# Performance work log

Measured on AMD Instinct MI355X. Metric: run time of the kernel, lower is better.

## Reference

```python
import jax, jax.numpy as jnp
import numpy as np

N, D_IN, D_OUT = 8192, 256, 256

def setup_inputs() -> dict:
    key = jax.random.key(0)
    k1, k2, k3, k4 = jax.random.split(key, 4)
    X = jax.random.normal(k1, (N, D_IN), dtype=jnp.float32)
    A = jax.random.uniform(k2, (N, N), dtype=jnp.float32)
    # nn.Linear params: weight (out, in) xavier-uniform, bias (out,)
    bound = float(np.sqrt(6.0 / (D_IN + D_OUT)))
    W = jax.random.uniform(k3, (D_OUT, D_IN), dtype=jnp.float32, minval=-bound, maxval=bound)
    b = jax.random.uniform(k4, (D_OUT,), dtype=jnp.float32, minval=-1.0 / np.sqrt(D_IN), maxval=1.0 / np.sqrt(D_IN))
    return {"X": X, "A": A, "W": W, "b": b}

def reference(X, A, W, b):
    n = A.shape[0]
    A2 = A + 2.0 * jnp.eye(n, dtype=A.dtype)          # A + 2I
    d = jnp.sum(A2, axis=1)                            # degree vector = diag(D)
    dis = jax.lax.rsqrt(d)                             # diag(D)^{-1/2} (diagonal inverse == reciprocal)
    A_norm = A2 * dis[:, None] * dis[None, :]          # D^{-1/2} A D^{-1/2} via row/col scaling
    AX = A_norm @ X                                    # (N, D_IN)
    out = jax.nn.relu(AX @ W.T + b)                    # Linear + ReLU
    return out
```

## Files before the change

### kernel.cpp

```cpp
#include <hip/hip_runtime.h>

#define N_ 8192
#define D_ 256

typedef short short8 __attribute__((ext_vector_type(8)));
typedef unsigned short u16x4 __attribute__((ext_vector_type(4)));
typedef unsigned short u16x8 __attribute__((ext_vector_type(8)));
typedef float f32x4 __attribute__((ext_vector_type(4)));

__device__ __forceinline__ unsigned short f2bf(float f) {
    union { float f; unsigned u; } v; v.f = f;
    unsigned r = v.u + 0x7FFFu + ((v.u >> 16) & 1u);
    return (unsigned short)(r >> 16);
}
__device__ __forceinline__ float bf2f(unsigned short h) {
    union { unsigned u; float f; } v; v.u = ((unsigned)h) << 16;
    return v.f;
}

__global__ __launch_bounds__(256) void k_dis(const float* __restrict__ A,
                                             float* __restrict__ disK) {
    const int w = threadIdx.x >> 6, l = threadIdx.x & 63;
    const int row = blockIdx.x * 4 + w;
    const float4* Ar = (const float4*)(A + (size_t)row * N_);
    float s = 0.f;
    #pragma unroll 8
    for (int i = l; i < N_ / 4; i += 64) {
        float4 v = Ar[i];
        s += (v.x + v.y) + (v.z + v.w);
    }
    #pragma unroll
    for (int o = 32; o; o >>= 1) s += __shfl_down(s, o);
    if (l == 0) disK[row] = rsqrtf(s + 2.0f);
}

__global__ __launch_bounds__(256) void k_P(
    const float* __restrict__ X, const float* __restrict__ W,
    const float* __restrict__ bv, const float* __restrict__ disK,
    unsigned short* __restrict__ Corr, unsigned short* __restrict__ Zt)
{
    __shared__ float sX[8][256];
    const int t = threadIdx.x;
    const int i0 = blockIdx.x * 8;

    {
        const int xr = t >> 5, xc = (t & 31) * 8;
        const float* src = X + (size_t)(i0 + xr) * D_ + xc;
        *(float4*)&sX[xr][xc]     = *(const float4*)(src);
        *(float4*)&sX[xr][xc + 4] = *(const float4*)(src + 4);
    }
    __syncthreads();

    const int c = t;
    float acc8[8];
    #pragma unroll
    for (int rr = 0; rr < 8; ++rr) acc8[rr] = 0.f;
    const float4* Wr = (const float4*)(W + (size_t)c * D_);
    for (int k4 = 0; k4 < 64; ++k4) {
        const float4 wv = Wr[k4];
        #pragma unroll
        for (int rr = 0; rr < 8; ++rr) {
            const float4 xv = *(const float4*)&sX[rr][k4 * 4];
            acc8[rr] += xv.x * wv.x + xv.y * wv.y + xv.z * wv.z + xv.w * wv.w;
        }
    }
    const float bc = bv[c];
    u16x8 zcol;
    #pragma unroll
    for (int rr = 0; rr < 8; ++rr) {
        const float p = acc8[rr];
        const float dv = disK[i0 + rr];
        Corr[(size_t)(i0 + rr) * D_ + c] = f2bf(2.0f * dv * dv * p + bc);
        zcol[rr] = f2bf(p);
    }
    *(u16x8*)(Zt + (size_t)c * N_ + i0) = zcol;
}

#define KBAR() do {                                             \
    asm volatile("s_waitcnt lgkmcnt(0)" ::: "memory");          \
    __builtin_amdgcn_sched_barrier(0);                          \
    __builtin_amdgcn_s_barrier();                               \
    __builtin_amdgcn_sched_barrier(0);                          \
} while (0)

__global__ __launch_bounds__(512) void kB(
    const float* __restrict__ A, const float* __restrict__ disK,
    const unsigned short* __restrict__ Corr, const unsigned short* __restrict__ Zt,
    float* __restrict__ out)
{
    __shared__ unsigned short sA[2][32][72];

    const int t = threadIdx.x, lane = t & 63, wid = t >> 6;
    const int m0 = blockIdx.x * 32, bn = wid * 32;

    const int sr = t >> 4, scq = t & 15;
    const float4* Ast = (const float4*)(A + (size_t)(m0 + sr) * N_) + scq;
    const float4* Dst = (const float4*)disK + scq;
    const unsigned short* Bq0 = Zt + (size_t)(bn + (lane & 15)) * N_ + (lane >> 4) * 8;
    const unsigned short* Bq1 = Bq0 + (size_t)16 * N_;

    f32x4 acc[2][2];
    #pragma unroll
    for (int m = 0; m < 2; ++m)
        #pragma unroll
        for (int n = 0; n < 2; ++n) acc[m][n] = (f32x4){0.f, 0.f, 0.f, 0.f};

    auto stage = [&](unsigned short (*buf)[72], float4 av, float4 dv) {
        u16x4 h;
        h[0] = f2bf(av.x * dv.x); h[1] = f2bf(av.y * dv.y);
        h[2] = f2bf(av.z * dv.z); h[3] = f2bf(av.w * dv.w);
        *(u16x4*)&buf[sr][scq * 4] = h;
    };
    auto loadB = [&](int ts, short8 (&bq)[2][2]) {
        const int k0 = ts * 64;
        bq[0][0] = *(const short8*)(Bq0 + k0);
        bq[0][1] = *(const short8*)(Bq0 + k0 + 32);
        bq[1][0] = *(const short8*)(Bq1 + k0);
        bq[1][1] = *(const short8*)(Bq1 + k0 + 32);
    };
    auto comp = [&](unsigned short (*buf)[72], short8 (&bq)[2][2]) {
        short8 af[2][2];
        #pragma unroll
        for (int mf = 0; mf < 2; ++mf)
            #pragma unroll
            for (int kk = 0; kk < 2; ++kk)
                af[mf][kk] = *(const short8*)&buf[mf * 16 + (lane & 15)]
                                                [kk * 32 + (lane >> 4) * 8];
        #pragma unroll
        for (int kk = 0; kk < 2; ++kk)
            #pragma unroll
            for (int mf = 0; mf < 2; ++mf)
                #pragma unroll
                for (int nf = 0; nf < 2; ++nf)
                    acc[mf][nf] = __builtin_amdgcn_mfma_f32_16x16x32_bf16(
                        af[mf][kk], bq[nf][kk], acc[mf][nf], 0, 0, 0);
    };

    float4 aA, aB, dA, dB;
    short8 bC[2][2], bN[2][2];

    {
        float4 l0 = Ast[0], d0 = Dst[0];
        aA = Ast[16]; dA = Dst[16];
        aB = Ast[32]; dB = Dst[32];
        loadB(0, bC);
        stage(sA[0], l0, d0);
        KBAR();
    }

    for (int t2 = 0; t2 < 64; ++t2) {
        const int ts = t2 * 2;
        stage(sA[1], aA, dA);
        { const int ka = min(ts + 3, 127); aA = Ast[ka * 16]; dA = Dst[ka * 16]; }
        loadB(min(ts + 1, 127), bN);
        comp(sA[0], bC);
        KBAR();
        stage(sA[0], aB, dB);
        { const int kb = min(ts + 4, 127); aB = Ast[kb * 16]; dB = Dst[kb * 16]; }
        loadB(min(ts + 2, 127), bC);
        comp(sA[1], bN);
        KBAR();
    }

    #pragma unroll
    for (int mf = 0; mf < 2; ++mf)
        #pragma unroll
        for (int r = 0; r < 4; ++r) {
            const int i = m0 + mf * 16 + ((lane >> 4) << 2) + r;
            const float dv = disK[i];
            #pragma unroll
            for (int nf = 0; nf < 2; ++nf) {
                const int c = bn + nf * 16 + (lane & 15);
                const float x = dv * acc[mf][nf][r] + bf2f(Corr[(size_t)i * D_ + c]);
                out[(size_t)i * D_ + c] = fmaxf(x, 0.f);
            }
        }
}

extern "C" void kernel_launch(void* const* d_in, const int* in_sizes, int n_in,
                              void* d_out, int out_size, void* d_ws, size_t ws_size,
                              hipStream_t stream) {
    (void)in_sizes; (void)n_in; (void)out_size; (void)ws_size;
    const float* X = (const float*)d_in[0];
    const float* A = (const float*)d_in[1];
    const float* W = (const float*)d_in[2];
    const float* b = (const float*)d_in[3];
    float* outp = (float*)d_out;

    float* disK = (float*)d_ws;
    unsigned short* Corr = (unsigned short*)((char*)d_ws + 32768);
    unsigned short* Zt   = Corr + (size_t)N_ * D_;

    k_dis<<<N_ / 4, 256, 0, stream>>>(A, disK);
    k_P<<<N_ / 8, 256, 0, stream>>>(X, W, b, disK, Corr, Zt);
    kB<<<N_ / 32, 512, 0, stream>>>(A, disK, Corr, Zt, outp);
}
```

Measured before the change: 211.5 us.

## Fold column scaling into Zt and deepen A/B prefetch pipeline to four stages

The column degree scaling dis[k] is moved from the streaming A tile conversion into the precomputed Zt operand, so kB no longer loads disK per step or multiplies A by it. The main loop becomes a four-buffer LDS ring with four in-flight A register loads, and B fragments are prefetched two steps ahead. A is read with nontemporal loads, and block order is reversed, probably to reuse the A rows still in cache from k_dis. This cuts per-step ALU work and hides more memory latency, at the cost of more registers and LDS, and it slightly changes rounding because dis*p is rounded to bf16.

```diff
diff --git a/kernel.cpp b/kernel.cpp
--- a/kernel.cpp
+++ b/kernel.cpp
@@ -71,7 +71,7 @@
         const float p = acc8[rr];
         const float dv = disK[i0 + rr];
         Corr[(size_t)(i0 + rr) * D_ + c] = f2bf(2.0f * dv * dv * p + bc);
-        zcol[rr] = f2bf(p);
+        zcol[rr] = f2bf(dv * p);
     }
     *(u16x8*)(Zt + (size_t)c * N_ + i0) = zcol;
 }
@@ -88,14 +88,14 @@
     const unsigned short* __restrict__ Corr, const unsigned short* __restrict__ Zt,
     float* __restrict__ out)
 {
-    __shared__ unsigned short sA[2][32][72];
+    __shared__ unsigned short sA[4][32][72];
 
     const int t = threadIdx.x, lane = t & 63, wid = t >> 6;
-    const int m0 = blockIdx.x * 32, bn = wid * 32;
+    const int m0 = (int)(gridDim.x - 1 - blockIdx.x) * 32;
+    const int bn = wid * 32;
 
     const int sr = t >> 4, scq = t & 15;
-    const float4* Ast = (const float4*)(A + (size_t)(m0 + sr) * N_) + scq;
-    const float4* Dst = (const float4*)disK + scq;
+    const f32x4* Ast = (const f32x4*)(A + (size_t)(m0 + sr) * N_) + scq;
     const unsigned short* Bq0 = Zt + (size_t)(bn + (lane & 15)) * N_ + (lane >> 4) * 8;
     const unsigned short* Bq1 = Bq0 + (size_t)16 * N_;
 
@@ -105,10 +105,14 @@
         #pragma unroll
         for (int n = 0; n < 2; ++n) acc[m][n] = (f32x4){0.f, 0.f, 0.f, 0.f};
 
-    auto stage = [&](unsigned short (*buf)[72], float4 av, float4 dv) {
-        u16x4 h;
-        h[0] = f2bf(av.x * dv.x); h[1] = f2bf(av.y * dv.y);
-        h[2] = f2bf(av.z * dv.z); h[3] = f2bf(av.w * dv.w);
+    f32x4 rA0, rA1, rA2, rA3;
+    short8 bq0[2][2], bq1[2][2], bq2[2][2], bq3[2][2];
+
+    auto ldA = [&](int ts) -> f32x4 {
+        return __builtin_nontemporal_load(Ast + (size_t)ts * 16);
+    };
+    auto stage = [&](unsigned short (*buf)[72], f32x4 v) {
+        u16x4 h; h[0]=f2bf(v[0]); h[1]=f2bf(v[1]); h[2]=f2bf(v[2]); h[3]=f2bf(v[3]);
         *(u16x4*)&buf[sr][scq * 4] = h;
     };
     auto loadB = [&](int ts, short8 (&bq)[2][2]) {
@@ -118,7 +122,7 @@
         bq[1][0] = *(const short8*)(Bq1 + k0);
         bq[1][1] = *(const short8*)(Bq1 + k0 + 32);
     };
-    auto comp = [&](unsigned short (*buf)[72], short8 (&bq)[2][2]) {
+    auto comp = [&](const unsigned short (*buf)[72], const short8 (&bq)[2][2]) {
         short8 af[2][2];
         #pragma unroll
         for (int mf = 0; mf < 2; ++mf)
@@ -136,31 +140,27 @@
                         af[mf][kk], bq[nf][kk], acc[mf][nf], 0, 0, 0);
     };
 
-    float4 aA, aB, dA, dB;
-    short8 bC[2][2], bN[2][2];
+    rA0 = ldA(0); rA1 = ldA(1); rA2 = ldA(2); rA3 = ldA(3);
+    loadB(0, bq0); loadB(1, bq1);
+    stage(sA[0], rA0);
+    KBAR();
 
-    {
-        float4 l0 = Ast[0], d0 = Dst[0];
-        aA = Ast[16]; dA = Dst[16];
-        aB = Ast[32]; dB = Dst[32];
-        loadB(0, bC);
-        stage(sA[0], l0, d0);
-        KBAR();
+#define KSTEP(TS, RAi, RAs, BSTG, BCMP, BQi, BQc) do {          \
+        RAi = ldA(min((TS) + 4, 127));                          \
+        stage(sA[BSTG], RAs);                                   \
+        loadB(min((TS) + 2, 127), BQi);                         \
+        comp(sA[BCMP], BQc);                                    \
+        KBAR();                                                 \
+    } while (0)
+
+    for (int it = 0; it < 32; ++it) {
+        const int ts = it * 4;
+        KSTEP(ts + 0, rA0, rA1, 1, 0, bq2, bq0);
+        KSTEP(ts + 1, rA1, rA2, 2, 1, bq3, bq1);
+        KSTEP(ts + 2, rA2, rA3, 3, 2, bq0, bq2);
+        KSTEP(ts + 3, rA3, rA0, 0, 3, bq1, bq3);
     }
-
-    for (int t2 = 0; t2 < 64; ++t2) {
-        const int ts = t2 * 2;
-        stage(sA[1], aA, dA);
-        { const int ka = min(ts + 3, 127); aA = Ast[ka * 16]; dA = Dst[ka * 16]; }
-        loadB(min(ts + 1, 127), bN);
-        comp(sA[0], bC);
-        KBAR();
-        stage(sA[0], aB, dB);
-        { const int kb = min(ts + 4, 127); aB = Ast[kb * 16]; dB = Dst[kb * 16]; }
-        loadB(min(ts + 2, 127), bC);
-        comp(sA[1], bN);
-        KBAR();
-    }
+#undef KSTEP
 
     #pragma unroll
     for (int mf = 0; mf < 2; ++mf)
```

New measurement: 215.0 us. About the same (+1.7%).

## Split-K main GEMM with 128-row tiles and separate reduction epilogue

Applied to the files above, without the earlier changes.

The main A·Z kernel now uses 128-row tiles with 4-way split-K over 2048-column ranges. Partial fp32 results are written to a workspace and summed by a new finalize kernel that applies the row scaling, correction term and ReLU. The column scaling by dis is folded into Zt in k_P, so A is converted straight to bf16 without a per-element multiply, and A is read with nontemporal loads. Each Zt tile is now reused across four times as many rows. In exchange, the change adds 32 MB of partial-sum traffic, an extra launch, and greater register pressure from 16 accumulator fragments.

```diff
diff --git a/kernel.cpp b/kernel.cpp
--- a/kernel.cpp
+++ b/kernel.cpp
@@ -2,6 +2,8 @@
 
 #define N_ 8192
 #define D_ 256
+#define KRANGE 2048
+#define BM 128
 
 typedef short short8 __attribute__((ext_vector_type(8)));
 typedef unsigned short u16x4 __attribute__((ext_vector_type(4)));
@@ -71,7 +73,7 @@
         const float p = acc8[rr];
         const float dv = disK[i0 + rr];
         Corr[(size_t)(i0 + rr) * D_ + c] = f2bf(2.0f * dv * dv * p + bc);
-        zcol[rr] = f2bf(p);
+        zcol[rr] = f2bf(dv * p);
     }
     *(u16x8*)(Zt + (size_t)c * N_ + i0) = zcol;
 }
@@ -84,97 +86,120 @@
 } while (0)
 
 __global__ __launch_bounds__(512) void kB(
-    const float* __restrict__ A, const float* __restrict__ disK,
-    const unsigned short* __restrict__ Corr, const unsigned short* __restrict__ Zt,
-    float* __restrict__ out)
+    const float* __restrict__ A, const unsigned short* __restrict__ Zt,
+    float* __restrict__ Cpart)
 {
-    __shared__ unsigned short sA[2][32][72];
+    __shared__ unsigned short sA[2][BM][72];
 
     const int t = threadIdx.x, lane = t & 63, wid = t >> 6;
-    const int m0 = blockIdx.x * 32, bn = wid * 32;
-
-    const int sr = t >> 4, scq = t & 15;
-    const float4* Ast = (const float4*)(A + (size_t)(m0 + sr) * N_) + scq;
-    const float4* Dst = (const float4*)disK + scq;
-    const unsigned short* Bq0 = Zt + (size_t)(bn + (lane & 15)) * N_ + (lane >> 4) * 8;
+    const int d = (int)blockIdx.x;
+    const int ks = (d & 7) >> 1;
+    const int mx = ((d >> 3) << 1) | (d & 1);
+    const int m0 = mx * BM;
+    const int kb = ks * KRANGE;
+    const int bn = wid * 32;
+
+    const int sr = t >> 2, sq = t & 3;
+    const float* Ast = A + (size_t)(m0 + sr) * N_ + kb + sq * 16;
+    const unsigned short* Bq0 = Zt + (size_t)(bn + (lane & 15)) * N_ + kb + (lane >> 4) * 8;
     const unsigned short* Bq1 = Bq0 + (size_t)16 * N_;
 
-    f32x4 acc[2][2];
-    #pragma unroll
-    for (int m = 0; m < 2; ++m)
+    f32x4 acc[8][2];
+    #pragma unroll
+    for (int m = 0; m < 8; ++m)
         #pragma unroll
         for (int n = 0; n < 2; ++n) acc[m][n] = (f32x4){0.f, 0.f, 0.f, 0.f};
 
-    auto stage = [&](unsigned short (*buf)[72], float4 av, float4 dv) {
-        u16x4 h;
-        h[0] = f2bf(av.x * dv.x); h[1] = f2bf(av.y * dv.y);
-        h[2] = f2bf(av.z * dv.z); h[3] = f2bf(av.w * dv.w);
-        *(u16x4*)&buf[sr][scq * 4] = h;
+    f32x4 s0[4], s1[4];
+    short8 bqA[2][2], bqB[2][2];
+
+    auto ldA4 = [&](f32x4 (&s)[4], int ts) {
+        const f32x4* p = (const f32x4*)(Ast + (size_t)min(ts, 31) * 64);
+        #pragma unroll
+        for (int j = 0; j < 4; ++j) s[j] = __builtin_nontemporal_load(p + j);
+    };
+    auto stage = [&](int buf, const f32x4 (&s)[4]) {
+        #pragma unroll
+        for (int j = 0; j < 4; ++j) {
+            u16x4 h; h[0]=f2bf(s[j][0]); h[1]=f2bf(s[j][1]);
+                     h[2]=f2bf(s[j][2]); h[3]=f2bf(s[j][3]);
+            *(u16x4*)&sA[buf][sr][sq * 16 + j * 4] = h;
+        }
     };
     auto loadB = [&](int ts, short8 (&bq)[2][2]) {
-        const int k0 = ts * 64;
+        const int k0 = min(ts, 31) * 64;
         bq[0][0] = *(const short8*)(Bq0 + k0);
         bq[0][1] = *(const short8*)(Bq0 + k0 + 32);
         bq[1][0] = *(const short8*)(Bq1 + k0);
         bq[1][1] = *(const short8*)(Bq1 + k0 + 32);
     };
-    auto comp = [&](unsigned short (*buf)[72], short8 (&bq)[2][2]) {
-        short8 af[2][2];
-        #pragma unroll
-        for (int mf = 0; mf < 2; ++mf)
+    auto comp = [&](int buf, const short8 (&bq)[2][2]) {
+        #pragma unroll
+        for (int mf = 0; mf < 8; ++mf) {
+            const short8 af0 = *(const short8*)&sA[buf][mf * 16 + (lane & 15)][(lane >> 4) * 8];
+            const short8 af1 = *(const short8*)&sA[buf][mf * 16 + (lane & 15)][32 + (lane >> 4) * 8];
             #pragma unroll
-            for (int kk = 0; kk < 2; ++kk)
-                af[mf][kk] = *(const short8*)&buf[mf * 16 + (lane & 15)]
-                                                [kk * 32 + (lane >> 4) * 8];
-        #pragma unroll
-        for (int kk = 0; kk < 2; ++kk)
-            #pragma unroll
-            for (int mf = 0; mf < 2; ++mf)
-                #pragma unroll
-                for (int nf = 0; nf < 2; ++nf)
-                    acc[mf][nf] = __builtin_amdgcn_mfma_f32_16x16x32_bf16(
-                        af[mf][kk], bq[nf][kk], acc[mf][nf], 0, 0, 0);
-    };
-
-    float4 aA, aB, dA, dB;
-    short8 bC[2][2], bN[2][2];
-
-    {
-        float4 l0 = Ast[0], d0 = Dst[0];
-        aA = Ast[16]; dA = Dst[16];
-        aB = Ast[32]; dB = Dst[32];
-        loadB(0, bC);
-        stage(sA[0], l0, d0);
+            for (int nf = 0; nf < 2; ++nf) {
+                acc[mf][nf] = __builtin_amdgcn_mfma_f32_16x16x32_bf16(
+                    af0, bq[nf][0], acc[mf][nf], 0, 0, 0);
+                acc[mf][nf] = __builtin_amdgcn_mfma_f32_16x16x32_bf16(
+                    af1, bq[nf][1], acc[mf][nf], 0, 0, 0);
+            }
+        }
+    };
+
+    ldA4(s0, 0); ldA4(s1, 1);
+    loadB(0, bqA);
+    stage(0, s0);
+    KBAR();
+
+    for (int it = 0; it < 16; ++it) {
+        const int ts = it * 2;
+        stage(1, s1);
+        ldA4(s0, ts + 2);
+        loadB(ts + 1, bqB);
+        comp(0, bqA);
         KBAR();
-    }
-
-    for (int t2 = 0; t2 < 64; ++t2) {
-        const int ts = t2 * 2;
-        stage(sA[1], aA, dA);
-        { const int ka = min(ts + 3, 127); aA = Ast[ka * 16]; dA = Dst[ka * 16]; }
-        loadB(min(ts + 1, 127), bN);
-        comp(sA[0], bC);
+        stage(0, s0);
+        ldA4(s1, ts + 3);
+        loadB(ts + 2, bqA);
+        comp(1, bqB);
         KBAR();
-        stage(sA[0], aB, dB);
-        { const int kb = min(ts + 4, 127); aB = Ast[kb * 16]; dB = Dst[kb * 16]; }
-        loadB(min(ts + 2, 127), bC);
-        comp(sA[1], bN);
-        KBAR();
-    }
-
-    #pragma unroll
-    for (int mf = 0; mf < 2; ++mf)
+    }
+
+    float* Cp = Cpart + (size_t)ks * ((size_t)N_ * D_);
+    #pragma unroll
+    for (int mf = 0; mf < 8; ++mf)
         #pragma unroll
         for (int r = 0; r < 4; ++r) {
             const int i = m0 + mf * 16 + ((lane >> 4) << 2) + r;
-            const float dv = disK[i];
             #pragma unroll
             for (int nf = 0; nf < 2; ++nf) {
                 const int c = bn + nf * 16 + (lane & 15);
-                const float x = dv * acc[mf][nf][r] + bf2f(Corr[(size_t)i * D_ + c]);
-                out[(size_t)i * D_ + c] = fmaxf(x, 0.f);
+                Cp[(size_t)i * D_ + c] = acc[mf][nf][r];
             }
         }
+}
+
+__global__ __launch_bounds__(256) void k_fin(
+    const float* __restrict__ Cpart, const float* __restrict__ disK,
+    const unsigned short* __restrict__ Corr, float* __restrict__ out)
+{
+    const size_t PL = (size_t)N_ * D_;
+    const int tid = blockIdx.x * 256 + threadIdx.x;
+    const size_t base = (size_t)tid * 4;
+    const int i = (int)(base >> 8);
+    const f32x4 p0 = *(const f32x4*)(Cpart + base);
+    const f32x4 p1 = *(const f32x4*)(Cpart + PL + base);
+    const f32x4 p2 = *(const f32x4*)(Cpart + 2 * PL + base);
+    const f32x4 p3 = *(const f32x4*)(Cpart + 3 * PL + base);
+    const u16x4 cr = *(const u16x4*)(Corr + base);
+    const float dv = disK[i];
+    f32x4 o;
+    #pragma unroll
+    for (int j = 0; j < 4; ++j)
+        o[j] = fmaxf(dv * ((p0[j] + p1[j]) + (p2[j] + p3[j])) + bf2f(cr[j]), 0.f);
+    *(f32x4*)(out + base) = o;
 }
 
 extern "C" void kernel_launch(void* const* d_in, const int* in_sizes, int n_in,
@@ -190,8 +215,10 @@
     float* disK = (float*)d_ws;
     unsigned short* Corr = (unsigned short*)((char*)d_ws + 32768);
     unsigned short* Zt   = Corr + (size_t)N_ * D_;
+    float* Cpart = (float*)((char*)d_ws + 32768 + 4 * (size_t)N_ * D_);
 
     k_dis<<<N_ / 4, 256, 0, stream>>>(A, disK);
     k_P<<<N_ / 8, 256, 0, stream>>>(X, W, b, disK, Corr, Zt);
-    kB<<<N_ / 32, 512, 0, stream>>>(A, disK, Corr, Zt, outp);
-}
+    kB<<<256, 512, 0, stream>>>(A, Zt, Cpart);
+    k_fin<<<(N_ * D_) / 1024, 256, 0, stream>>>(Cpart, disK, Corr, outp);
+}
```

Result: faster. 195.2 us (-7.7%).
